# Kernel tuning notes

Measured on AMD Instinct MI355X. Metric: run time of the kernel, lower is better.

Reference implementation:

```python
import jax, jax.numpy as jnp
import numpy as np

RX = 49
R = 1.0
ANGLES = [-10.0, 0.0, 10.0]


def _make_kernels(rx, r, angles_deg):
    # same construction as the torch __init__
    angles = np.rad2deg(np.arctan(r * np.tan(np.deg2rad(np.asarray(angles_deg, np.float64)))))
    ks = []
    for A in angles:
        lval = np.arange(rx) - rx // 2
        lval = np.round(lval * np.tan(np.deg2rad(A))).astype(np.int32)
        ry = (lval.max() - lval.min()) // 2 * 2 + 1
        i, _ = np.meshgrid(np.arange(ry), np.arange(rx))
        i = i - ry // 2
        k = (i == lval[:, None]).astype(np.float32)[None, None]  # [1,1,rx,ry], one nonzero per row
        ks.append(k)
    return ks

_KERNELS = [jnp.asarray(k) for k in _make_kernels(RX, R, ANGLES)]
_PADS = [(int(k.shape[2]) // 2, int(k.shape[3]) // 2) for k in _KERNELS]  # (pc, pr)


def _boxfilter(x, k, pc, pr):
    # torch.conv2d(F.pad(x,(pr,pr,pc,pc)), k) == cross-correlation with symmetric zero pad
    return jax.lax.conv_general_dilated(x, k, (1, 1), ((pc, pc), (pr, pr)),
                                        dimension_numbers=('NCHW', 'OIHW', 'NCHW'))


def _reflect(x, size):
    # PyTorch reflection padding for align_corners=True: reflect about [0, size-1]
    span = size - 1
    if span <= 0:
        return jnp.zeros_like(x)
    ax = jnp.abs(x)
    extra = jnp.mod(ax, span)
    flips = jnp.floor(ax / span)
    out = jnp.where(jnp.mod(flips, 2.0) == 0.0, extra, span - extra)
    return jnp.clip(out, 0.0, span)


def _grid_sample(x, grid):
    # bilinear, padding_mode='reflection', align_corners=True; x:[B,C,H,W], grid:[B,Hg,Wg,2]
    B, C, H, W = x.shape
    gx = _reflect((grid[..., 0] + 1.0) * 0.5 * (W - 1), W)
    gy = _reflect((grid[..., 1] + 1.0) * 0.5 * (H - 1), H)
    x0 = jnp.floor(gx)
    y0 = jnp.floor(gy)
    wx = gx - x0
    wy = gy - y0
    xi0 = jnp.clip(x0, 0, W - 1).astype(jnp.int32)
    yi0 = jnp.clip(y0, 0, H - 1).astype(jnp.int32)
    xi1 = jnp.clip(x0 + 1.0, 0, W - 1).astype(jnp.int32)
    yi1 = jnp.clip(y0 + 1.0, 0, H - 1).astype(jnp.int32)
    gather = jax.vmap(lambda img, yi, xi: img[:, yi, xi])  # [B,C,Hg,Wg]
    v00 = gather(x, yi0, xi0)
    v01 = gather(x, yi0, xi1)
    v10 = gather(x, yi1, xi0)
    v11 = gather(x, yi1, xi1)
    wx = wx[:, None]  # [B,1,Hg,Wg] broadcast over channel
    wy = wy[:, None]
    return (v00 * (1 - wx) * (1 - wy) + v01 * wx * (1 - wy)
            + v10 * (1 - wx) * wy + v11 * wx * wy)


def setup_inputs() -> dict:
    key = jax.random.key(0)
    k1, k2, k3, k4 = jax.random.split(key, 4)
    B, H, W = 1, 2048, 2048
    X = jax.random.uniform(k1, (B, 1, H, W), jnp.float32)
    y = jax.random.uniform(k2, (B, 1, H, W), jnp.float32)
    hX = jax.random.normal(k3, (B, 1, H, W), jnp.float32)
    coor = jax.random.uniform(k4, (B, H, W, 2), jnp.float32, minval=-1.0, maxval=1.0)
    return {"X": X, "y": y, "hX": hX, "coor": coor}


def reference(X, y, hX, coor):
    # N: normalization = boxfilter of ones (computed once per shape in torch; recomputed here)
    N = [_boxfilter(jnp.ones_like(X), k, pc, pr) for k, (pc, pr) in zip(_KERNELS, _PADS)]
    X0 = X
    Xc = X
    for (k, (pc, pr)), Ni in zip(zip(_KERNELS, _PADS), N):
        b = _boxfilter(y - Xc, k, pc, pr) / Ni
        b = _boxfilter(b, k, pc, pr) / Ni
        Xc = Xc + b
    return _grid_sample(Xc - X0, coor) + hX
```

## Files before the change

kernel.cpp:

```cpp
#include <hip/hip_runtime.h>
#include <hip/hip_fp16.h>

static constexpr int HH = 2048;
static constexpr int WW = 2048;
static constexpr int PADT = 24;
static constexpr int PADL = 8;
static constexpr int SW   = WW + 2 * PADL;
static constexpr int PROWS = HH + 2 * PADT;
static constexpr size_t PadElems = (size_t)PROWS * SW;
static constexpr int RS = 8;
static constexpr int RV = 16;

__device__ constexpr int CS[9] = {-24,-19,-14,-8,-2, 3, 9,15,20};
__device__ constexpr int CE[9] = {-20,-15, -9,-3, 2, 8,14,19,24};
__device__ constexpr int CO[9] = { -4, -3, -2,-1, 0, 1, 2, 3, 4};

__device__ __forceinline__ void swz_s(int& bx, int& by) {
  const int bid = blockIdx.x;
  const int xcd = bid & 7, i = bid >> 3;
  by = xcd * 32 + (i & 31);
  bx = i >> 5;
}
__device__ __forceinline__ void swz_v(int& bx, int& by) {
  const int bid = blockIdx.x;
  const int xcd = bid & 7, i = bid >> 3;
  by = xcd * 16 + (i & 15);
  bx = i >> 4;
}

template<int SS, int EE, int OO, int NROWS>
__device__ __forceinline__ void seg_one(const __half* __restrict__ tp, int h0, int w,
                                        float* __restrict__ acc) {
  constexpr int L = EE - SS + 1;
  const __half* p = tp + (h0 + SS + PADT) * SW + (w + OO + PADL);
  float ring[L - 1];
  float s = 0.0f;
#pragma unroll
  for (int k = 0; k < L - 1; ++k) { float v = __half2float(p[k * SW]); ring[k] = v; s += v; }
#pragma unroll
  for (int r = 0; r < NROWS; ++r) {
    float v = __half2float(p[(L - 1 + r) * SW]);
    acc[r] += s + v;
    s += v - ring[r % (L - 1)];
    ring[r % (L - 1)] = v;
  }
}

template<int SGN, int NROWS>
__device__ __forceinline__ void filt_slant(const __half* __restrict__ tp, int h0, int w,
                                           float* __restrict__ acc) {
#pragma unroll
  for (int r = 0; r < NROWS; ++r) acc[r] = 0.0f;
  seg_one<-24, -20, -4 * SGN, NROWS>(tp, h0, w, acc);
  seg_one<-19, -15, -3 * SGN, NROWS>(tp, h0, w, acc);
  seg_one<-14,  -9, -2 * SGN, NROWS>(tp, h0, w, acc);
  seg_one< -8,  -3, -1 * SGN, NROWS>(tp, h0, w, acc);
  seg_one< -2,   2,  0      , NROWS>(tp, h0, w, acc);
  seg_one<  3,   8,  1 * SGN, NROWS>(tp, h0, w, acc);
  seg_one<  9,  14,  2 * SGN, NROWS>(tp, h0, w, acc);
  seg_one< 15,  19,  3 * SGN, NROWS>(tp, h0, w, acc);
  seg_one< 20,  24,  4 * SGN, NROWS>(tp, h0, w, acc);
}

template<int A>
__device__ __forceinline__ float rcpcnt(int h, int w) {
  if (h >= 24 && h <= 2023 && w >= 4 && w <= 2043) return 1.0f / 49.0f;
  int cnt = 0;
  const int sgn = (A == 0) ? -1 : 1;
#pragma unroll
  for (int j = 0; j < 9; ++j) {
    const int ww = w + sgn * CO[j];
    const int ov = min(h + CE[j], HH - 1) - max(h + CS[j], 0) + 1;
    if (ww >= 0 && ww < WW && ov > 0) cnt += ov;
  }
  return 1.0f / (float)cnt;
}

__device__ __forceinline__ float rcpcnt1(int h) {
  return 1.0f / (float)(min(h + 24, HH - 1) - max(h - 24, 0) + 1);
}

template<int A>
__global__ __launch_bounds__(256) void passA(const __half* __restrict__ tcur,
                                             __half* __restrict__ bp) {
  int bx, by; swz_s(bx, by);
  const int w  = bx * 256 + threadIdx.x;
  const int h0 = by * RS;
  float acc[RS];
  filt_slant<(A == 0) ? -1 : 1, RS>(tcur, h0, w, acc);
#pragma unroll
  for (int r = 0; r < RS; ++r) {
    const int h = h0 + r;
    bp[(h + PADT) * SW + (w + PADL)] = __float2half(acc[r] * rcpcnt<A>(h, w));
  }
}

template<int A>
__global__ __launch_bounds__(256) void passB(const __half* __restrict__ bp,
                                             __half* __restrict__ tcur) {
  int bx, by; swz_s(bx, by);
  const int w  = bx * 256 + threadIdx.x;
  const int h0 = by * RS;
  float acc[RS];
  filt_slant<(A == 0) ? -1 : 1, RS>(bp, h0, w, acc);
#pragma unroll
  for (int r = 0; r < RS; ++r) {
    const int h = h0 + r;
    const size_t ip = (size_t)(h + PADT) * SW + (w + PADL);
    tcur[ip] = __float2half(__half2float(tcur[ip]) - acc[r] * rcpcnt<A>(h, w));
  }
}

__global__ __launch_bounds__(256) void passA1v(const __half* __restrict__ tcur,
                                               __half* __restrict__ bp) {
  int bx, by; swz_v(bx, by);
  const int w2 = (bx * 256 + threadIdx.x) * 2;
  const int h0 = by * RV;
  const size_t st = SW / 2;
  const __half2* p = (const __half2*)(tcur + (size_t)(h0 - 24 + PADT) * SW) + (w2 + PADL) / 2;
  float sx = 0.0f, sy = 0.0f;
#pragma unroll
  for (int k = 0; k < 48; ++k) {
    const float2 v = __half22float2(p[k * st]); sx += v.x; sy += v.y;
  }
#pragma unroll
  for (int r = 0; r < RV; ++r) {
    const int h = h0 + r;
    const float2 vin = __half22float2(p[(48 + r) * st]);
    const float rc = rcpcnt1(h);
    __half2* o = (__half2*)(bp + (size_t)(h + PADT) * SW + (w2 + PADL));
    *o = __floats2half2_rn((sx + vin.x) * rc, (sy + vin.y) * rc);
    const float2 vout = __half22float2(p[r * st]);
    sx += vin.x - vout.x; sy += vin.y - vout.y;
  }
}

__global__ __launch_bounds__(256) void passB1v(const __half* __restrict__ bp,
                                               __half* __restrict__ tcur) {
  int bx, by; swz_v(bx, by);
  const int w2 = (bx * 256 + threadIdx.x) * 2;
  const int h0 = by * RV;
  const size_t st = SW / 2;
  const __half2* p = (const __half2*)(bp + (size_t)(h0 - 24 + PADT) * SW) + (w2 + PADL) / 2;
  float sx = 0.0f, sy = 0.0f;
#pragma unroll
  for (int k = 0; k < 48; ++k) {
    const float2 v = __half22float2(p[k * st]); sx += v.x; sy += v.y;
  }
#pragma unroll
  for (int r = 0; r < RV; ++r) {
    const int h = h0 + r;
    const float2 vin = __half22float2(p[(48 + r) * st]);
    const float rc = rcpcnt1(h);
    __half2* o = (__half2*)(tcur + (size_t)(h + PADT) * SW + (w2 + PADL));
    const float2 cur = __half22float2(*o);
    *o = __floats2half2_rn(cur.x - (sx + vin.x) * rc, cur.y - (sy + vin.y) * rc);
    const float2 vout = __half22float2(p[r * st]);
    sx += vin.x - vout.x; sy += vin.y - vout.y;
  }
}

template<int A>
__global__ __launch_bounds__(256) void passBF(const __half* __restrict__ bp,
                                              __half* __restrict__ tcur,
                                              const __half* __restrict__ t0h,
                                              unsigned int* __restrict__ scaleU) {
  int bx, by; swz_s(bx, by);
  const int w  = bx * 256 + threadIdx.x;
  const int h0 = by * RS;
  float acc[RS];
  filt_slant<(A == 0) ? -1 : 1, RS>(bp, h0, w, acc);
  float m = 0.0f;
#pragma unroll
  for (int r = 0; r < RS; ++r) {
    const int h = h0 + r;
    const size_t i  = (size_t)h * WW + w;
    const size_t ip = (size_t)(h + PADT) * SW + (w + PADL);
    const float res = __half2float(t0h[i]) - __half2float(tcur[ip]) +
                      acc[r] * rcpcnt<A>(h, w);
    tcur[ip] = __float2half(res);
    m = fmaxf(m, fabsf(res));
  }
#pragma unroll
  for (int off = 32; off >= 1; off >>= 1) m = fmaxf(m, __shfl_xor(m, off));
  __shared__ float red[4];
  if ((threadIdx.x & 63) == 0) red[threadIdx.x >> 6] = m;
  __syncthreads();
  if (threadIdx.x == 0) {
    const float bm = fmaxf(fmaxf(red[0], red[1]), fmaxf(red[2], red[3]));
    atomicMax(scaleU, __float_as_uint(bm));
  }
}

__global__ __launch_bounds__(256) void quantV8(const __half* __restrict__ tcur,
                                               const unsigned int* __restrict__ scaleU,
                                               unsigned long long* __restrict__ V8) {
  const int i = blockIdx.x * 256 + threadIdx.x;
  const int s = i >> 11, x = i & (WW - 1);
  const float mg = __uint_as_float(*scaleU);
  const float inv = (mg > 0.0f) ? 127.0f / mg : 0.0f;
  const __half* base = tcur + (size_t)(8 * s + PADT) * SW + (x + PADL);
  unsigned long long v = 0;
#pragma unroll
  for (int j = 0; j < 8; ++j) {
    const float f = __half2float(base[(size_t)j * SW]);
    const int q = min(max((int)rintf(f * inv), -127), 127);
    v |= (unsigned long long)(unsigned char)(q & 0xff) << (8 * j);
  }
  V8[i] = v;
}

__global__ __launch_bounds__(64) void zeropad(__half* __restrict__ tp, __half* __restrict__ bp,
                                              unsigned int* __restrict__ scaleU) {
  if (blockIdx.x == 0 && blockIdx.y == 0 && threadIdx.x == 0) *scaleU = 0u;
  __half* buf = blockIdx.y ? bp : tp;
  const int row = blockIdx.x;
  __half* r = buf + (size_t)row * SW;
  const __half z = __float2half(0.0f);
  if (row < PADT || row >= PADT + HH) {
    for (int c = threadIdx.x; c < SW; c += 64) r[c] = z;
  } else if (threadIdx.x < PADL) {
    r[threadIdx.x] = z;
    r[PADL + WW + threadIdx.x] = z;
  }
}

__global__ __launch_bounds__(256) void sub2pad(const float* __restrict__ y,
                                               const float* __restrict__ X,
                                               __half* __restrict__ tcur,
                                               __half* __restrict__ t0h) {
  const int i = blockIdx.x * 256 + threadIdx.x;
  const int p = i * 4;
  const int h = p >> 11, w = p & (WW - 1);
  const float4 Y = ((const float4*)y)[i];
  const float4 Xv = ((const float4*)X)[i];
  union { __half2 h2; unsigned u; } a, b;
  a.h2 = __floats2half2_rn(Y.x - Xv.x, Y.y - Xv.y);
  b.h2 = __floats2half2_rn(Y.z - Xv.z, Y.w - Xv.w);
  uint2 o; o.x = a.u; o.y = b.u;
  *(uint2*)(tcur + (size_t)(h + PADT) * SW + (w + PADL)) = o;
  *(uint2*)(t0h + (size_t)p) = o;
}

__global__ __launch_bounds__(256) void gather_k(const unsigned long long* __restrict__ V8,
                                                const unsigned int* __restrict__ scaleU,
                                                const unsigned long long* __restrict__ coorU,
                                                const float* __restrict__ hX,
                                                float* __restrict__ out) {
  const int i = blockIdx.x * 256 + threadIdx.x;
  const unsigned long long cu = __builtin_nontemporal_load(&coorU[i]);
  union { unsigned long long u; float f[2]; } cc; cc.u = cu;
  const float gx = fminf(fmaxf((cc.f[0] + 1.0f) * 0.5f * (float)(WW - 1), 0.0f), (float)(WW - 1));
  const float gy = fminf(fmaxf((cc.f[1] + 1.0f) * 0.5f * (float)(HH - 1), 0.0f), (float)(HH - 1));
  const float x0 = floorf(gx), y0 = floorf(gy);
  const float wx = gx - x0, wy = gy - y0;
  const int xi0 = min(max((int)x0, 0), WW - 1);
  const int xi1 = min(xi0 + 1, WW - 1);
  const int yi0 = min(max((int)y0, 0), HH - 1);
  const int yi1 = min(max((int)(y0 + 1.0f), 0), HH - 1);
  const int s0 = yi0 >> 3, s1 = yi1 >> 3;
  const int j0 = (yi0 & 7) * 8, j1 = (yi1 & 7) * 8;
  const unsigned long long c00 = V8[(size_t)s0 * WW + xi0];
  const unsigned long long c01 = V8[(size_t)s0 * WW + xi1];
  unsigned long long c10 = c00, c11 = c01;
  if (s1 != s0) {
    c10 = V8[(size_t)s1 * WW + xi0];
    c11 = V8[(size_t)s1 * WW + xi1];
  }
  const float v00 = (float)(signed char)(c00 >> j0);
  const float v01 = (float)(signed char)(c01 >> j0);
  const float v10 = (float)(signed char)(c10 >> j1);
  const float v11 = (float)(signed char)(c11 >> j1);
  const float sc = __uint_as_float(*scaleU) * (1.0f / 127.0f);
  const float hx = __builtin_nontemporal_load(&hX[i]);
  const float bil = v00 * (1.0f - wx) * (1.0f - wy) + v01 * wx * (1.0f - wy) +
                    v10 * (1.0f - wx) * wy + v11 * wx * wy;
  __builtin_nontemporal_store(bil * sc + hx, &out[i]);
}

extern "C" void kernel_launch(void* const* d_in, const int* in_sizes, int n_in,
                              void* d_out, int out_size, void* d_ws, size_t ws_size,
                              hipStream_t stream) {
  const float* X    = (const float*)d_in[0];
  const float* y    = (const float*)d_in[1];
  const float* hX   = (const float*)d_in[2];
  const float* coor = (const float*)d_in[3];
  float* out = (float*)d_out;

  __half* tcur = (__half*)d_ws;
  __half* bp   = tcur + PadElems;
  __half* t0h  = bp + PadElems;
  unsigned long long* V8 = (unsigned long long*)(t0h + (size_t)HH * WW);
  unsigned int* scaleU = (unsigned int*)(V8 + (size_t)(HH / 8) * WW);

  const int n = HH * WW;
  const int sblocks = (WW / 256) * (HH / RS);
  const int vblocks = (WW / 512) * (HH / RV);

  zeropad<<<dim3(PROWS, 2, 1), 64, 0, stream>>>(tcur, bp, scaleU);
  sub2pad<<<(n / 4) / 256, 256, 0, stream>>>(y, X, tcur, t0h);

  passA<0><<<sblocks, 256, 0, stream>>>(tcur, bp);
  passB<0><<<sblocks, 256, 0, stream>>>(bp, tcur);
  passA1v<<<vblocks, 256, 0, stream>>>(tcur, bp);
  passB1v<<<vblocks, 256, 0, stream>>>(bp, tcur);
  passA<2><<<sblocks, 256, 0, stream>>>(tcur, bp);
  passBF<2><<<sblocks, 256, 0, stream>>>(bp, tcur, t0h, scaleU);

  quantV8<<<(n / 8) / 256, 256, 0, stream>>>(tcur, scaleU, V8);
  gather_k<<<n / 256, 256, 0, stream>>>(V8, scaleU, (const unsigned long long*)coor, hX, out);
}
```

Before: 163.1 us.

## Process two columns per thread with packed half2 accumulation in slant filters

The slanted box-filter passes now have each thread handle two adjacent columns. Loads are 32-bit half2, and odd column offsets are realigned with shifts from two neighbouring words. The running sums and the ring buffer use packed fp16 arithmetic instead of fp32, and the vertical passes and the quantisation kernel get the same two-column packing. This halves the thread count and the load instructions and doubles math throughput, at the cost of fp16 accumulation error in 49-tap running sums and extra unaligned-word loads.

```diff
diff --git a/kernel.cpp b/kernel.cpp
--- a/kernel.cpp
+++ b/kernel.cpp
@@ -8,14 +8,18 @@
 static constexpr int SW   = WW + 2 * PADL;
 static constexpr int PROWS = HH + 2 * PADT;
 static constexpr size_t PadElems = (size_t)PROWS * SW;
-static constexpr int RS = 8;
+static constexpr int RSP = 8;
 static constexpr int RV = 16;
 
 __device__ constexpr int CS[9] = {-24,-19,-14,-8,-2, 3, 9,15,20};
 __device__ constexpr int CE[9] = {-20,-15, -9,-3, 2, 8,14,19,24};
 __device__ constexpr int CO[9] = { -4, -3, -2,-1, 0, 1, 2, 3, 4};
 
-__device__ __forceinline__ void swz_s(int& bx, int& by) {
+union U32H2 { unsigned u; __half2 h; };
+__device__ __forceinline__ __half2 u2h(unsigned u) { U32H2 x; x.u = u; return x.h; }
+__device__ __forceinline__ unsigned h2u(__half2 h) { U32H2 x; x.h = h; return x.u; }
+
+__device__ __forceinline__ void swz_s2(int& bx, int& by) {
   const int bid = blockIdx.x;
   const int xcd = bid & 7, i = bid >> 3;
   by = xcd * 32 + (i & 31);
@@ -29,37 +33,49 @@
 }
 
 template<int SS, int EE, int OO, int NROWS>
-__device__ __forceinline__ void seg_one(const __half* __restrict__ tp, int h0, int w,
-                                        float* __restrict__ acc) {
-  constexpr int L = EE - SS + 1;
-  const __half* p = tp + (h0 + SS + PADT) * SW + (w + OO + PADL);
-  float ring[L - 1];
-  float s = 0.0f;
-#pragma unroll
-  for (int k = 0; k < L - 1; ++k) { float v = __half2float(p[k * SW]); ring[k] = v; s += v; }
+__device__ __forceinline__ void seg2p(const __half* __restrict__ tp, int h0, int w2,
+                                      __half2* __restrict__ acc) {
+  constexpr int NR = EE - SS;
+  constexpr bool EVEN = ((OO & 1) == 0);
+  const size_t st = SW / 2;
+  const unsigned* p = (const unsigned*)(tp + (size_t)(h0 + SS + PADT) * SW +
+                                        (w2 + PADL + (EVEN ? OO : OO - 1)));
+  unsigned ring[NR];
+  __half2 s = u2h(0u);
+#pragma unroll
+  for (int k = 0; k < NR; ++k) {
+    unsigned u;
+    if constexpr (EVEN) { u = p[k * st]; }
+    else { const unsigned ul = p[k * st], ur = p[k * st + 1]; u = (ul >> 16) | (ur << 16); }
+    ring[k] = u;
+    s = __hadd2(s, u2h(u));
+  }
 #pragma unroll
   for (int r = 0; r < NROWS; ++r) {
-    float v = __half2float(p[(L - 1 + r) * SW]);
-    acc[r] += s + v;
-    s += v - ring[r % (L - 1)];
-    ring[r % (L - 1)] = v;
+    unsigned u;
+    if constexpr (EVEN) { u = p[(NR + r) * st]; }
+    else { const unsigned ul = p[(NR + r) * st], ur = p[(NR + r) * st + 1]; u = (ul >> 16) | (ur << 16); }
+    const __half2 v = u2h(u);
+    acc[r] = __hadd2(acc[r], __hadd2(s, v));
+    s = __hadd2(s, __hsub2(v, u2h(ring[r % NR])));
+    ring[r % NR] = u;
   }
 }
 
 template<int SGN, int NROWS>
-__device__ __forceinline__ void filt_slant(const __half* __restrict__ tp, int h0, int w,
-                                           float* __restrict__ acc) {
-#pragma unroll
-  for (int r = 0; r < NROWS; ++r) acc[r] = 0.0f;
-  seg_one<-24, -20, -4 * SGN, NROWS>(tp, h0, w, acc);
-  seg_one<-19, -15, -3 * SGN, NROWS>(tp, h0, w, acc);
-  seg_one<-14,  -9, -2 * SGN, NROWS>(tp, h0, w, acc);
-  seg_one< -8,  -3, -1 * SGN, NROWS>(tp, h0, w, acc);
-  seg_one< -2,   2,  0      , NROWS>(tp, h0, w, acc);
-  seg_one<  3,   8,  1 * SGN, NROWS>(tp, h0, w, acc);
-  seg_one<  9,  14,  2 * SGN, NROWS>(tp, h0, w, acc);
-  seg_one< 15,  19,  3 * SGN, NROWS>(tp, h0, w, acc);
-  seg_one< 20,  24,  4 * SGN, NROWS>(tp, h0, w, acc);
+__device__ __forceinline__ void filt_slant2p(const __half* __restrict__ tp, int h0, int w2,
+                                             __half2* __restrict__ acc) {
+#pragma unroll
+  for (int r = 0; r < NROWS; ++r) acc[r] = u2h(0u);
+  seg2p<-24, -20, -4 * SGN, NROWS>(tp, h0, w2, acc);
+  seg2p<-19, -15, -3 * SGN, NROWS>(tp, h0, w2, acc);
+  seg2p<-14,  -9, -2 * SGN, NROWS>(tp, h0, w2, acc);
+  seg2p< -8,  -3, -1 * SGN, NROWS>(tp, h0, w2, acc);
+  seg2p< -2,   2,  0      , NROWS>(tp, h0, w2, acc);
+  seg2p<  3,   8,  1 * SGN, NROWS>(tp, h0, w2, acc);
+  seg2p<  9,  14,  2 * SGN, NROWS>(tp, h0, w2, acc);
+  seg2p< 15,  19,  3 * SGN, NROWS>(tp, h0, w2, acc);
+  seg2p< 20,  24,  4 * SGN, NROWS>(tp, h0, w2, acc);
 }
 
 template<int A>
@@ -83,80 +99,36 @@
 template<int A>
 __global__ __launch_bounds__(256) void passA(const __half* __restrict__ tcur,
                                              __half* __restrict__ bp) {
-  int bx, by; swz_s(bx, by);
-  const int w  = bx * 256 + threadIdx.x;
-  const int h0 = by * RS;
-  float acc[RS];
-  filt_slant<(A == 0) ? -1 : 1, RS>(tcur, h0, w, acc);
-#pragma unroll
-  for (int r = 0; r < RS; ++r) {
-    const int h = h0 + r;
-    bp[(h + PADT) * SW + (w + PADL)] = __float2half(acc[r] * rcpcnt<A>(h, w));
+  int bx, by; swz_s2(bx, by);
+  const int w2 = (bx * 256 + threadIdx.x) * 2;
+  const int h0 = by * RSP;
+  __half2 acc[RSP];
+  filt_slant2p<(A == 0) ? -1 : 1, RSP>(tcur, h0, w2, acc);
+#pragma unroll
+  for (int r = 0; r < RSP; ++r) {
+    const int h = h0 + r;
+    const float2 f = __half22float2(acc[r]);
+    *(unsigned*)(bp + (size_t)(h + PADT) * SW + (w2 + PADL)) =
+        h2u(__floats2half2_rn(f.x * rcpcnt<A>(h, w2), f.y * rcpcnt<A>(h, w2 + 1)));
   }
 }
 
 template<int A>
 __global__ __launch_bounds__(256) void passB(const __half* __restrict__ bp,
                                              __half* __restrict__ tcur) {
-  int bx, by; swz_s(bx, by);
-  const int w  = bx * 256 + threadIdx.x;
-  const int h0 = by * RS;
-  float acc[RS];
-  filt_slant<(A == 0) ? -1 : 1, RS>(bp, h0, w, acc);
-#pragma unroll
-  for (int r = 0; r < RS; ++r) {
-    const int h = h0 + r;
-    const size_t ip = (size_t)(h + PADT) * SW + (w + PADL);
-    tcur[ip] = __float2half(__half2float(tcur[ip]) - acc[r] * rcpcnt<A>(h, w));
-  }
-}
-
-__global__ __launch_bounds__(256) void passA1v(const __half* __restrict__ tcur,
-                                               __half* __restrict__ bp) {
-  int bx, by; swz_v(bx, by);
-  const int w2 = (bx * 256 + threadIdx.x) * 2;
-  const int h0 = by * RV;
-  const size_t st = SW / 2;
-  const __half2* p = (const __half2*)(tcur + (size_t)(h0 - 24 + PADT) * SW) + (w2 + PADL) / 2;
-  float sx = 0.0f, sy = 0.0f;
-#pragma unroll
-  for (int k = 0; k < 48; ++k) {
-    const float2 v = __half22float2(p[k * st]); sx += v.x; sy += v.y;
-  }
-#pragma unroll
-  for (int r = 0; r < RV; ++r) {
-    const int h = h0 + r;
-    const float2 vin = __half22float2(p[(48 + r) * st]);
-    const float rc = rcpcnt1(h);
-    __half2* o = (__half2*)(bp + (size_t)(h + PADT) * SW + (w2 + PADL));
-    *o = __floats2half2_rn((sx + vin.x) * rc, (sy + vin.y) * rc);
-    const float2 vout = __half22float2(p[r * st]);
-    sx += vin.x - vout.x; sy += vin.y - vout.y;
-  }
-}
-
-__global__ __launch_bounds__(256) void passB1v(const __half* __restrict__ bp,
-                                               __half* __restrict__ tcur) {
-  int bx, by; swz_v(bx, by);
-  const int w2 = (bx * 256 + threadIdx.x) * 2;
-  const int h0 = by * RV;
-  const size_t st = SW / 2;
-  const __half2* p = (const __half2*)(bp + (size_t)(h0 - 24 + PADT) * SW) + (w2 + PADL) / 2;
-  float sx = 0.0f, sy = 0.0f;
-#pragma unroll
-  for (int k = 0; k < 48; ++k) {
-    const float2 v = __half22float2(p[k * st]); sx += v.x; sy += v.y;
-  }
-#pragma unroll
-  for (int r = 0; r < RV; ++r) {
-    const int h = h0 + r;
-    const float2 vin = __half22float2(p[(48 + r) * st]);
-    const float rc = rcpcnt1(h);
-    __half2* o = (__half2*)(tcur + (size_t)(h + PADT) * SW + (w2 + PADL));
-    const float2 cur = __half22float2(*o);
-    *o = __floats2half2_rn(cur.x - (sx + vin.x) * rc, cur.y - (sy + vin.y) * rc);
-    const float2 vout = __half22float2(p[r * st]);
-    sx += vin.x - vout.x; sy += vin.y - vout.y;
+  int bx, by; swz_s2(bx, by);
+  const int w2 = (bx * 256 + threadIdx.x) * 2;
+  const int h0 = by * RSP;
+  __half2 acc[RSP];
+  filt_slant2p<(A == 0) ? -1 : 1, RSP>(bp, h0, w2, acc);
+#pragma unroll
+  for (int r = 0; r < RSP; ++r) {
+    const int h = h0 + r;
+    unsigned* o = (unsigned*)(tcur + (size_t)(h + PADT) * SW + (w2 + PADL));
+    const float2 cur = __half22float2(u2h(*o));
+    const float2 f = __half22float2(acc[r]);
+    *o = h2u(__floats2half2_rn(cur.x - f.x * rcpcnt<A>(h, w2),
+                               cur.y - f.y * rcpcnt<A>(h, w2 + 1)));
   }
 }
 
@@ -165,21 +137,23 @@
                                               __half* __restrict__ tcur,
                                               const __half* __restrict__ t0h,
                                               unsigned int* __restrict__ scaleU) {
-  int bx, by; swz_s(bx, by);
-  const int w  = bx * 256 + threadIdx.x;
-  const int h0 = by * RS;
-  float acc[RS];
-  filt_slant<(A == 0) ? -1 : 1, RS>(bp, h0, w, acc);
+  int bx, by; swz_s2(bx, by);
+  const int w2 = (bx * 256 + threadIdx.x) * 2;
+  const int h0 = by * RSP;
+  __half2 acc[RSP];
+  filt_slant2p<(A == 0) ? -1 : 1, RSP>(bp, h0, w2, acc);
   float m = 0.0f;
 #pragma unroll
-  for (int r = 0; r < RS; ++r) {
-    const int h = h0 + r;
-    const size_t i  = (size_t)h * WW + w;
-    const size_t ip = (size_t)(h + PADT) * SW + (w + PADL);
-    const float res = __half2float(t0h[i]) - __half2float(tcur[ip]) +
-                      acc[r] * rcpcnt<A>(h, w);
-    tcur[ip] = __float2half(res);
-    m = fmaxf(m, fabsf(res));
+  for (int r = 0; r < RSP; ++r) {
+    const int h = h0 + r;
+    const float2 t0 = __half22float2(u2h(*(const unsigned*)(t0h + (size_t)h * WW + w2)));
+    unsigned* o = (unsigned*)(tcur + (size_t)(h + PADT) * SW + (w2 + PADL));
+    const float2 cur = __half22float2(u2h(*o));
+    const float2 f = __half22float2(acc[r]);
+    const float rx = t0.x - cur.x + f.x * rcpcnt<A>(h, w2);
+    const float ry = t0.y - cur.y + f.y * rcpcnt<A>(h, w2 + 1);
+    *o = h2u(__floats2half2_rn(rx, ry));
+    m = fmaxf(m, fmaxf(fabsf(rx), fabsf(ry)));
   }
 #pragma unroll
   for (int off = 32; off >= 1; off >>= 1) m = fmaxf(m, __shfl_xor(m, off));
@@ -192,22 +166,71 @@
   }
 }
 
+__global__ __launch_bounds__(256) void passA1v(const __half* __restrict__ tcur,
+                                               __half* __restrict__ bp) {
+  int bx, by; swz_v(bx, by);
+  const int w2 = (bx * 256 + threadIdx.x) * 2;
+  const int h0 = by * RV;
+  const size_t st = SW / 2;
+  const unsigned* p = (const unsigned*)(tcur + (size_t)(h0 - 24 + PADT) * SW + (w2 + PADL));
+  __half2 s = u2h(0u);
+#pragma unroll
+  for (int k = 0; k < 48; ++k) s = __hadd2(s, u2h(p[k * st]));
+#pragma unroll
+  for (int r = 0; r < RV; ++r) {
+    const int h = h0 + r;
+    const __half2 vin = u2h(p[(48 + r) * st]);
+    const float2 f = __half22float2(__hadd2(s, vin));
+    const float rc = rcpcnt1(h);
+    *(unsigned*)(bp + (size_t)(h + PADT) * SW + (w2 + PADL)) =
+        h2u(__floats2half2_rn(f.x * rc, f.y * rc));
+    s = __hadd2(s, __hsub2(vin, u2h(p[r * st])));
+  }
+}
+
+__global__ __launch_bounds__(256) void passB1v(const __half* __restrict__ bp,
+                                               __half* __restrict__ tcur) {
+  int bx, by; swz_v(bx, by);
+  const int w2 = (bx * 256 + threadIdx.x) * 2;
+  const int h0 = by * RV;
+  const size_t st = SW / 2;
+  const unsigned* p = (const unsigned*)(bp + (size_t)(h0 - 24 + PADT) * SW + (w2 + PADL));
+  __half2 s = u2h(0u);
+#pragma unroll
+  for (int k = 0; k < 48; ++k) s = __hadd2(s, u2h(p[k * st]));
+#pragma unroll
+  for (int r = 0; r < RV; ++r) {
+    const int h = h0 + r;
+    const __half2 vin = u2h(p[(48 + r) * st]);
+    const float2 f = __half22float2(__hadd2(s, vin));
+    const float rc = rcpcnt1(h);
+    unsigned* o = (unsigned*)(tcur + (size_t)(h + PADT) * SW + (w2 + PADL));
+    const float2 cur = __half22float2(u2h(*o));
+    *o = h2u(__floats2half2_rn(cur.x - f.x * rc, cur.y - f.y * rc));
+    s = __hadd2(s, __hsub2(vin, u2h(p[r * st])));
+  }
+}
+
 __global__ __launch_bounds__(256) void quantV8(const __half* __restrict__ tcur,
                                                const unsigned int* __restrict__ scaleU,
                                                unsigned long long* __restrict__ V8) {
   const int i = blockIdx.x * 256 + threadIdx.x;
-  const int s = i >> 11, x = i & (WW - 1);
+  const int s = i >> 10, x2 = (i & 1023) * 2;
   const float mg = __uint_as_float(*scaleU);
   const float inv = (mg > 0.0f) ? 127.0f / mg : 0.0f;
-  const __half* base = tcur + (size_t)(8 * s + PADT) * SW + (x + PADL);
-  unsigned long long v = 0;
+  const unsigned* base = (const unsigned*)(tcur + (size_t)(8 * s + PADT) * SW + (x2 + PADL));
+  const size_t st = SW / 2;
+  unsigned long long va = 0, vb = 0;
 #pragma unroll
   for (int j = 0; j < 8; ++j) {
-    const float f = __half2float(base[(size_t)j * SW]);
-    const int q = min(max((int)rintf(f * inv), -127), 127);
-    v |= (unsigned long long)(unsigned char)(q & 0xff) << (8 * j);
-  }
-  V8[i] = v;
+    const float2 f = __half22float2(u2h(base[(size_t)j * st]));
+    const int qa = min(max((int)rintf(f.x * inv), -127), 127);
+    const int qb = min(max((int)rintf(f.y * inv), -127), 127);
+    va |= (unsigned long long)(unsigned char)(qa & 0xff) << (8 * j);
+    vb |= (unsigned long long)(unsigned char)(qb & 0xff) << (8 * j);
+  }
+  unsigned long long* o = V8 + (size_t)s * WW + x2;
+  o[0] = va; o[1] = vb;
 }
 
 __global__ __launch_bounds__(64) void zeropad(__half* __restrict__ tp, __half* __restrict__ bp,
@@ -294,7 +317,7 @@
   unsigned int* scaleU = (unsigned int*)(V8 + (size_t)(HH / 8) * WW);
 
   const int n = HH * WW;
-  const int sblocks = (WW / 256) * (HH / RS);
+  const int sblocks = (WW / 512) * (HH / RSP);
   const int vblocks = (WW / 512) * (HH / RV);
 
   zeropad<<<dim3(PROWS, 2, 1), 64, 0, stream>>>(tcur, bp, scaleU);
@@ -307,6 +330,6 @@
   passA<2><<<sblocks, 256, 0, stream>>>(tcur, bp);
   passBF<2><<<sblocks, 256, 0, stream>>>(bp, tcur, t0h, scaleU);
 
-  quantV8<<<(n / 8) / 256, 256, 0, stream>>>(tcur, scaleU, V8);
+  quantV8<<<((HH / 8) * (WW / 2)) / 256, 256, 0, stream>>>(tcur, scaleU, V8);
   gather_k<<<n / 256, 256, 0, stream>>>(V8, scaleU, (const unsigned long long*)coor, hX, out);
 }
```

Measured after the change: 147.3 us. 1.11x faster.
